# Kernel optimization log

Measured on AMD Instinct MI355X. Metric: run time of the kernel, lower is better.

## Reference

```python
import jax, jax.numpy as jnp
import numpy as np

B, S, D, H = 4, 2048, 1024, 16
HD = D // H

def setup_inputs() -> dict:
    key = jax.random.key(0)
    ks = jax.random.split(key, 5)
    x = jax.random.normal(ks[0], (B, S, D), dtype=jnp.float32)
    mask = jnp.ones((B, S), dtype=jnp.int32)
    # torch nn.Linear init scale ~ 1/sqrt(fan_in); use small normal for stability
    qkv_w = jax.random.normal(ks[1], (3 * D, D), dtype=jnp.float32) * (1.0 / np.sqrt(D))
    qkv_b = jax.random.normal(ks[2], (3 * D,), dtype=jnp.float32) * 0.02
    out_w = jax.random.normal(ks[3], (D, D), dtype=jnp.float32) * (1.0 / np.sqrt(D))
    out_b = jax.random.normal(ks[4], (D,), dtype=jnp.float32) * 0.02
    return {"x": x, "mask": mask, "qkv_w": qkv_w, "qkv_b": qkv_b,
            "out_w": out_w, "out_b": out_b}

def reference(x, mask, qkv_w, qkv_b, out_w, out_b):
    b, s, d = x.shape
    scale = np.sqrt(HD).astype(np.float32)
    # qkv projection: torch Linear y = x @ W^T + b
    qkv = x @ qkv_w.T + qkv_b                      # (b, s, 3d)
    qkv = qkv.reshape(b, s, 3, H, HD)
    qkv = jnp.transpose(qkv, (2, 0, 3, 1, 4))      # (3, b, H, s, hd)
    q, k, v = qkv[0], qkv[1], qkv[2]
    scores = jnp.einsum('bhqd,bhkd->bhqk', q, k) / scale  # (b, H, s, s)
    neg_inf = jnp.float32(-jnp.inf)
    causal = jnp.tril(jnp.ones((s, s), dtype=bool))
    scores = jnp.where(causal[None, None], scores, neg_inf)
    key_mask = (mask != 0)[:, None, None, :]       # (b, 1, 1, s)
    scores = jnp.where(key_mask, scores, neg_inf)
    attn = jax.nn.softmax(scores, axis=-1)
    out = jnp.einsum('bhqk,bhkd->bhqd', attn, v)   # (b, H, s, hd)
    out = jnp.transpose(out, (0, 2, 1, 3)).reshape(b, s, d)
    return out @ out_w.T + out_b
```

## Files before the change

kernel.cpp:

```cpp
#include <hip/hip_runtime.h>
#include <stdint.h>
#include <type_traits>

#define BB  4
#define SS  2048
#define DD  1024
#define HH  16
#define HDD 64

typedef __attribute__((ext_vector_type(8))) short s16x8;
typedef __attribute__((ext_vector_type(4))) float f32x4;

__device__ inline short f2bf(float f) {
    union { float f; unsigned int u; } v; v.f = f;
    unsigned int r = (v.u + 0x7fffu + ((v.u >> 16) & 1u)) >> 16;
    return (short)r;
}

#define GLL(gp, lp) __builtin_amdgcn_global_load_lds( \
    (const __attribute__((address_space(1))) void*)(gp), \
    (__attribute__((address_space(3))) void*)(lp), 16, 0, 0)

__global__ void cvt_kernel(const float* __restrict__ src, short* __restrict__ dst, int n) {
    int i = (blockIdx.x * 256 + threadIdx.x) * 8;
    if (i >= n) return;
    const float4* s = (const float4*)(src + i);
    float4 a = s[0], b = s[1];
    s16x8 o;
    o[0]=f2bf(a.x); o[1]=f2bf(a.y); o[2]=f2bf(a.z); o[3]=f2bf(a.w);
    o[4]=f2bf(b.x); o[5]=f2bf(b.y); o[6]=f2bf(b.z); o[7]=f2bf(b.w);
    *(s16x8*)(dst + i) = o;
}

template<int EPI>
__global__ __launch_bounds__(256)
void gemm_bt(const short* __restrict__ A, const short* __restrict__ Bw,
             const float* __restrict__ bias, float* __restrict__ Cf,
             short* __restrict__ Qo, short* __restrict__ Ko, short* __restrict__ Vo,
             int M, int N, int K)
{
    __shared__ short lsA[128 * 32];
    __shared__ short lsB[128 * 32];
    const int tid  = threadIdx.x;
    const int w    = tid >> 6, lane = tid & 63;
    const int quad = lane >> 4, l15 = lane & 15;
    const int m0 = blockIdx.x * 128, n0 = blockIdx.y * 128;
    const int mw = (w & 1) * 64, nw = (w >> 1) * 64;

    f32x4 acc[4][4] = {};

    const int srow = w * 32 + (lane >> 2);
    const int scol = (lane & 3) * 8;
    const short* pA = A + (size_t)(m0 + srow) * K + scol;
    const short* pB = Bw + (size_t)(n0 + srow) * K + scol;
    short* lAbase0 = &lsA[(w * 32) * 32];
    short* lAbase1 = &lsA[(w * 32 + 16) * 32];
    short* lBbase0 = &lsB[(w * 32) * 32];
    short* lBbase1 = &lsB[(w * 32 + 16) * 32];

    for (int kk = 0; kk < K; kk += 32) {
        __syncthreads();
        GLL(pA + kk,            lAbase0);
        GLL(pA + kk + 16 * K,   lAbase1);
        GLL(pB + kk,            lBbase0);
        GLL(pB + kk + 16 * K,   lBbase1);
        asm volatile("s_waitcnt vmcnt(0)" ::: "memory");
        __syncthreads();

        s16x8 af[4], bfr[4];
        for (int t = 0; t < 4; ++t) {
            af[t]  = *(const s16x8*)&lsA[(mw + t * 16 + l15) * 32 + quad * 8];
            bfr[t] = *(const s16x8*)&lsB[(nw + t * 16 + l15) * 32 + quad * 8];
        }
        for (int i = 0; i < 4; ++i)
            for (int j = 0; j < 4; ++j)
                acc[i][j] = __builtin_amdgcn_mfma_f32_16x16x32_bf16(af[i], bfr[j], acc[i][j], 0, 0, 0);
    }

    if (EPI == 0) {
        for (int i = 0; i < 4; ++i) {
            int row = m0 + mw + i * 16 + quad * 4;
            for (int j = 0; j < 4; ++j) {
                int col = n0 + nw + j * 16 + l15;
                float bv = bias[col];
                for (int r = 0; r < 4; ++r)
                    Cf[(size_t)(row + r) * N + col] = acc[i][j][r] + bv;
            }
        }
    } else {
        for (int i = 0; i < 4; ++i) {
            int row = m0 + mw + i * 16 + quad * 4;
            for (int j = 0; j < 4; ++j) {
                int col = n0 + nw + j * 16 + l15;
                float bv = bias[col];
                int sel = col >> 10, h = (col >> 6) & 15, hd = col & 63;
                for (int r = 0; r < 4; ++r) {
                    int rr = row + r;
                    int b = rr >> 11, s = rr & 2047;
                    short val = f2bf(acc[i][j][r] + bv);
                    if (sel == 0)      Qo[(((size_t)b * HH + h) * SS + s) * HDD + hd] = val;
                    else if (sel == 1) Ko[(((size_t)b * HH + h) * SS + s) * HDD + hd] = val;
                    else               Vo[(((size_t)b * HH + h) * HDD + hd) * SS + s] = val;
                }
            }
        }
    }
}

__global__ __launch_bounds__(256, 4)
void attn_kernel(const short* __restrict__ Q, const short* __restrict__ Kb,
                 const short* __restrict__ Vb, const int* __restrict__ mask,
                 short* __restrict__ O)
{
    __shared__ short lsK[128 * 72];
    __shared__ short lsV[64 * 136];
    __shared__ float lsM[128];

    const int tid  = threadIdx.x;
    const int w    = tid >> 6, lane = tid & 63;
    const int quad = lane >> 4, l15 = lane & 15;
    const int bx = blockIdx.x, bh = blockIdx.y;
    const int b = bh >> 4;
    const size_t baseQK = (size_t)bh * SS * HDD;
    const size_t baseV  = (size_t)bh * HDD * SS;
    short* lsPw = &lsK[w * 16 * 136];
    const float SC = 0.18033688f;

    for (int t = 0; t < 2; ++t) {
        const int qb = t ? bx : (31 - bx);
        const int q0 = qb * 64;
        const int qrow = q0 + w * 16 + l15;
        const int rowg0 = q0 + w * 16 + quad * 4;

        s16x8 aq[2];
        for (int ks = 0; ks < 2; ++ks)
            aq[ks] = *(const s16x8*)(Q + baseQK + (size_t)qrow * HDD + ks * 32 + quad * 8);

        float m_r[4], l_r[4];
        f32x4 o_acc[4] = {};
        for (int r = 0; r < 4; ++r) { m_r[r] = -1e30f; l_r[r] = 0.f; }

        auto tile = [&](auto NTC, auto CC, int kv0) {
            constexpr int NT     = decltype(NTC)::value;
            constexpr bool CAUS  = decltype(CC)::value;
            __syncthreads();
            for (int i = 0; i < NT / 2; ++i) {
                int ch = tid + i * 256;
                int row = ch >> 3, cs = (ch & 7) * 8;
                *(s16x8*)&lsK[row * 72 + cs] =
                    *(const s16x8*)(Kb + baseQK + (size_t)(kv0 + row) * HDD + cs);
            }
            if constexpr (NT == 8) {
                for (int i = 0; i < 4; ++i) {
                    int ch = tid + i * 256;
                    int row = ch >> 4, cs = (ch & 15) * 8;
                    *(s16x8*)&lsV[row * 136 + cs] =
                        *(const s16x8*)(Vb + baseV + (size_t)row * SS + kv0 + cs);
                }
            } else {
                for (int i = 0; i < 2; ++i) {
                    int ch = tid + i * 256;
                    int row = ch >> 3, cs = (ch & 7) * 8;
                    *(s16x8*)&lsV[row * 136 + cs] =
                        *(const s16x8*)(Vb + baseV + (size_t)row * SS + kv0 + cs);
                }
            }
            if (tid < NT * 16) lsM[tid] = (mask[b * SS + kv0 + tid] != 0) ? 0.f : -1e30f;
            __syncthreads();

            f32x4 sv[NT];
            for (int nt = 0; nt < NT; ++nt) {
                f32x4 s = {};
                for (int ks = 0; ks < 2; ++ks) {
                    s16x8 kf = *(const s16x8*)&lsK[(nt * 16 + l15) * 72 + ks * 32 + quad * 8];
                    s = __builtin_amdgcn_mfma_f32_16x16x32_bf16(aq[ks], kf, s, 0, 0, 0);
                }
                sv[nt] = s;
            }
            for (int nt = 0; nt < NT; ++nt) {
                int colg = kv0 + nt * 16 + l15;
                float madd = lsM[nt * 16 + l15];
                for (int r = 0; r < 4; ++r) {
                    float scv = sv[nt][r] * SC + madd;
                    if (CAUS && colg > rowg0 + r) scv = -1e30f;
                    sv[nt][r] = scv;
                }
            }
            float alpha[4];
            for (int r = 0; r < 4; ++r) {
                float rm = sv[0][r];
                for (int nt = 1; nt < NT; ++nt) rm = fmaxf(rm, sv[nt][r]);
                rm = fmaxf(rm, __shfl_xor(rm, 1));
                rm = fmaxf(rm, __shfl_xor(rm, 2));
                rm = fmaxf(rm, __shfl_xor(rm, 4));
                rm = fmaxf(rm, __shfl_xor(rm, 8));
                float nm = fmaxf(m_r[r], rm);
                alpha[r] = __builtin_amdgcn_exp2f(m_r[r] - nm);
                m_r[r] = nm;
                float rs = 0.f;
                for (int nt = 0; nt < NT; ++nt) {
                    float p = __builtin_amdgcn_exp2f(sv[nt][r] - nm);
                    sv[nt][r] = p;
                    rs += p;
                }
                rs += __shfl_xor(rs, 1);
                rs += __shfl_xor(rs, 2);
                rs += __shfl_xor(rs, 4);
                rs += __shfl_xor(rs, 8);
                l_r[r] = l_r[r] * alpha[r] + rs;
            }
            for (int ht = 0; ht < 4; ++ht)
                for (int r = 0; r < 4; ++r)
                    o_acc[ht][r] *= alpha[r];

            __syncthreads();
            for (int nt = 0; nt < NT; ++nt)
                for (int r = 0; r < 4; ++r)
                    lsPw[(quad * 4 + r) * 136 + nt * 16 + l15] = f2bf(sv[nt][r]);
            asm volatile("s_waitcnt lgkmcnt(0)" ::: "memory");

            for (int k2 = 0; k2 < NT / 2; ++k2) {
                s16x8 ap = *(const s16x8*)&lsPw[l15 * 136 + k2 * 32 + quad * 8];
                for (int ht = 0; ht < 4; ++ht) {
                    s16x8 vf = *(const s16x8*)&lsV[(ht * 16 + l15) * 136 + k2 * 32 + quad * 8];
                    o_acc[ht] = __builtin_amdgcn_mfma_f32_16x16x32_bf16(ap, vf, o_acc[ht], 0, 0, 0);
                }
            }
        };

        const int nfull = q0 / 128;
        for (int kt = 0; kt < nfull; ++kt)
            tile(std::integral_constant<int, 8>{}, std::false_type{}, kt * 128);
        if (qb & 1) tile(std::integral_constant<int, 8>{}, std::true_type{}, nfull * 128);
        else        tile(std::integral_constant<int, 4>{}, std::true_type{}, nfull * 128);

        const int hcol = (bh & 15) * HDD;
        for (int r = 0; r < 4; ++r) {
            float inv = 1.0f / l_r[r];
            int srow = q0 + w * 16 + quad * 4 + r;
            size_t base = ((size_t)b * SS + srow) * DD + hcol;
            for (int ht = 0; ht < 4; ++ht)
                O[base + ht * 16 + l15] = f2bf(o_acc[ht][r] * inv);
        }
    }
}

extern "C" void kernel_launch(void* const* d_in, const int* in_sizes, int n_in,
                              void* d_out, int out_size, void* d_ws, size_t ws_size,
                              hipStream_t stream) {
    const float* x     = (const float*)d_in[0];
    const int*   mask  = (const int*)d_in[1];
    const float* qkv_w = (const float*)d_in[2];
    const float* qkv_b = (const float*)d_in[3];
    const float* out_w = (const float*)d_in[4];
    const float* out_b = (const float*)d_in[5];
    float* out = (float*)d_out;

    const size_t M1 = (size_t)BB * SS;
    short* ws  = (short*)d_ws;
    short* xb  = ws;
    short* qwb = xb  + M1 * DD;
    short* owb = qwb + (size_t)3 * DD * DD;
    short* Qb  = owb + (size_t)DD * DD;
    short* Kb  = Qb  + M1 * DD;
    short* Vb  = Kb  + M1 * DD;
    short* Ob  = Vb  + M1 * DD;

    cvt_kernel<<<(int)(M1 * DD / 8 / 256), 256, 0, stream>>>(x, xb, (int)(M1 * DD));
    cvt_kernel<<<3 * DD * DD / 8 / 256, 256, 0, stream>>>(qkv_w, qwb, 3 * DD * DD);
    cvt_kernel<<<DD * DD / 8 / 256, 256, 0, stream>>>(out_w, owb, DD * DD);

    gemm_bt<1><<<dim3(64, 24), 256, 0, stream>>>(xb, qwb, qkv_b, nullptr,
                                                 Qb, Kb, Vb, 8192, 3072, 1024);
    attn_kernel<<<dim3(16, BB * HH), 256, 0, stream>>>(Qb, Kb, Vb, mask, Ob);
    gemm_bt<0><<<dim3(64, 8), 256, 0, stream>>>(Ob, owb, out_b, out,
                                                nullptr, nullptr, nullptr, 8192, 1024, 1024);
}
```

Measured before the change: 323.0 us.

## Load K/V fragments directly from global memory, drop shared staging and block barriers

The attention kernel no longer stages K and V tiles (and the mask) in LDS behind __syncthreads. Each wave now reads its MFMA K and V operands straight from global memory, with the loads batched ahead of the MFMAs. The mask is read per lane, and the per-wave P buffer gets an XOR swizzle to cut bank conflicts. This removes block-wide synchronisation and LDS traffic, and smaller shared memory may allow more occupancy. The cost is that every wave re-reads K/V from global/L2 instead of sharing them through LDS.

Result: slower. 476.1 us (+47.4%).

```diff
diff --git a/kernel.cpp b/kernel.cpp
--- a/kernel.cpp
+++ b/kernel.cpp
@@ -112,9 +112,7 @@
                  const short* __restrict__ Vb, const int* __restrict__ mask,
                  short* __restrict__ O)
 {
-    __shared__ short lsK[128 * 72];
-    __shared__ short lsV[64 * 136];
-    __shared__ float lsM[128];
+    __shared__ short lsP[4][16 * 136];
 
     const int tid  = threadIdx.x;
     const int w    = tid >> 6, lane = tid & 63;
@@ -123,8 +121,10 @@
     const int b = bh >> 4;
     const size_t baseQK = (size_t)bh * SS * HDD;
     const size_t baseV  = (size_t)bh * HDD * SS;
-    short* lsPw = &lsK[w * 16 * 136];
+    short* lsPw = lsP[w];
     const float SC = 0.18033688f;
+    const int rsw = (l15 >> 3) << 4;
+    const int wsw = (quad >> 1) << 4;
 
     for (int t = 0; t < 2; ++t) {
         const int qb = t ? bx : (31 - bx);
@@ -143,45 +143,27 @@
         auto tile = [&](auto NTC, auto CC, int kv0) {
             constexpr int NT     = decltype(NTC)::value;
             constexpr bool CAUS  = decltype(CC)::value;
-            __syncthreads();
-            for (int i = 0; i < NT / 2; ++i) {
-                int ch = tid + i * 256;
-                int row = ch >> 3, cs = (ch & 7) * 8;
-                *(s16x8*)&lsK[row * 72 + cs] =
-                    *(const s16x8*)(Kb + baseQK + (size_t)(kv0 + row) * HDD + cs);
-            }
-            if constexpr (NT == 8) {
-                for (int i = 0; i < 4; ++i) {
-                    int ch = tid + i * 256;
-                    int row = ch >> 4, cs = (ch & 15) * 8;
-                    *(s16x8*)&lsV[row * 136 + cs] =
-                        *(const s16x8*)(Vb + baseV + (size_t)row * SS + kv0 + cs);
-                }
-            } else {
-                for (int i = 0; i < 2; ++i) {
-                    int ch = tid + i * 256;
-                    int row = ch >> 3, cs = (ch & 7) * 8;
-                    *(s16x8*)&lsV[row * 136 + cs] =
-                        *(const s16x8*)(Vb + baseV + (size_t)row * SS + kv0 + cs);
-                }
-            }
-            if (tid < NT * 16) lsM[tid] = (mask[b * SS + kv0 + tid] != 0) ? 0.f : -1e30f;
-            __syncthreads();
-
-            f32x4 sv[NT];
-            for (int nt = 0; nt < NT; ++nt) {
-                f32x4 s = {};
-                for (int ks = 0; ks < 2; ++ks) {
-                    s16x8 kf = *(const s16x8*)&lsK[(nt * 16 + l15) * 72 + ks * 32 + quad * 8];
-                    s = __builtin_amdgcn_mfma_f32_16x16x32_bf16(aq[ks], kf, s, 0, 0, 0);
-                }
-                sv[nt] = s;
-            }
+
+            float madd[NT];
+            for (int nt = 0; nt < NT; ++nt)
+                madd[nt] = (mask[b * SS + kv0 + nt * 16 + l15] != 0) ? 0.f : -1e30f;
+
+            const short* Kp = Kb + baseQK + (size_t)(kv0 + l15) * HDD + quad * 8;
+            f32x4 sv[NT] = {};
+            for (int ks = 0; ks < 2; ++ks) {
+                for (int c = 0; c < NT; c += 4) {
+                    s16x8 kf[4];
+                    for (int u = 0; u < 4; ++u)
+                        kf[u] = *(const s16x8*)(Kp + (size_t)(c + u) * 16 * HDD + ks * 32);
+                    for (int u = 0; u < 4; ++u)
+                        sv[c + u] = __builtin_amdgcn_mfma_f32_16x16x32_bf16(aq[ks], kf[u], sv[c + u], 0, 0, 0);
+                }
+            }
+
             for (int nt = 0; nt < NT; ++nt) {
                 int colg = kv0 + nt * 16 + l15;
-                float madd = lsM[nt * 16 + l15];
                 for (int r = 0; r < 4; ++r) {
-                    float scv = sv[nt][r] * SC + madd;
+                    float scv = sv[nt][r] * SC + madd[nt];
                     if (CAUS && colg > rowg0 + r) scv = -1e30f;
                     sv[nt][r] = scv;
                 }
@@ -213,18 +195,22 @@
                 for (int r = 0; r < 4; ++r)
                     o_acc[ht][r] *= alpha[r];
 
-            __syncthreads();
             for (int nt = 0; nt < NT; ++nt)
                 for (int r = 0; r < 4; ++r)
-                    lsPw[(quad * 4 + r) * 136 + nt * 16 + l15] = f2bf(sv[nt][r]);
+                    lsPw[((quad * 4 + r) * 136 + nt * 16 + l15) ^ wsw] = f2bf(sv[nt][r]);
             asm volatile("s_waitcnt lgkmcnt(0)" ::: "memory");
-
-            for (int k2 = 0; k2 < NT / 2; ++k2) {
-                s16x8 ap = *(const s16x8*)&lsPw[l15 * 136 + k2 * 32 + quad * 8];
-                for (int ht = 0; ht < 4; ++ht) {
-                    s16x8 vf = *(const s16x8*)&lsV[(ht * 16 + l15) * 136 + k2 * 32 + quad * 8];
-                    o_acc[ht] = __builtin_amdgcn_mfma_f32_16x16x32_bf16(ap, vf, o_acc[ht], 0, 0, 0);
-                }
+            __builtin_amdgcn_sched_barrier(0);
+
+            s16x8 ap[NT / 2];
+            for (int k2 = 0; k2 < NT / 2; ++k2)
+                ap[k2] = *(const s16x8*)&lsPw[(l15 * 136 + k2 * 32 + quad * 8) ^ rsw];
+            const short* Vp = Vb + baseV + kv0 + quad * 8;
+            for (int ht = 0; ht < 4; ++ht) {
+                s16x8 vf[NT / 2];
+                for (int k2 = 0; k2 < NT / 2; ++k2)
+                    vf[k2] = *(const s16x8*)(Vp + (size_t)(ht * 16 + l15) * SS + k2 * 32);
+                for (int k2 = 0; k2 < NT / 2; ++k2)
+                    o_acc[ht] = __builtin_amdgcn_mfma_f32_16x16x32_bf16(ap[k2], vf[k2], o_acc[ht], 0, 0, 0);
             }
         };
 
```
